# Optimization experiments

Hardware: AMD Instinct MI355X
Metric: run time of the kernel (lower is better)

The kernel has to match this reference:

```python
import jax, jax.numpy as jnp
import numpy as np

NEG_SLOPE = 0.2
MASK_FILL = -1e9

N, F_IN, K, F_OUT = 4096, 512, 8, 128


def setup_inputs() -> dict:
    key = jax.random.key(0)
    k1, k2, k3, k4, k5 = jax.random.split(key, 5)
    x = jax.random.normal(k1, (N, F_IN), dtype=jnp.float32)
    mask = jax.random.randint(k2, (N, N), 0, 2).astype(jnp.bool_)
    # ensure no fully-masked row (self loops)
    mask = mask | jnp.eye(N, dtype=jnp.bool_)
    # xavier-ish scaled params
    W = jax.random.normal(k3, (K * F_OUT, F_IN), dtype=jnp.float32) * (2.0 / (F_IN + K * F_OUT)) ** 0.5
    b = jnp.zeros((K * F_OUT,), dtype=jnp.float32)
    a_left = jax.random.normal(k4, (K, F_OUT), dtype=jnp.float32) * (2.0 / (1 + F_OUT)) ** 0.5
    a_right = jax.random.normal(k5, (K, F_OUT), dtype=jnp.float32) * (2.0 / (1 + F_OUT)) ** 0.5
    return {"x": x, "mask": mask, "W": W, "b": b, "a_left": a_left, "a_right": a_right}


def reference(x, mask, W, b, a_left, a_right):
    # Linear projection: (N, K*F') -> (N, K, F')
    h = (x @ W.T + b).reshape(x.shape[0], K, F_OUT)
    # Additive attention logits: e[k,n,m] = leaky_relu(a_left.h_n + a_right.h_m)
    left = jnp.einsum('nkf,kf->kn', h, a_left)    # (K, N)
    right = jnp.einsum('mkf,kf->km', h, a_right)  # (K, N)
    e = jax.nn.leaky_relu(left[:, :, None] + right[:, None, :], NEG_SLOPE)  # (K,N,N)
    # Mask out non-neighbors, softmax over neighbor axis m
    e = jnp.where(mask[None, :, :], e, MASK_FILL)
    a = jax.nn.softmax(e, axis=-1)  # (K, N, N)
    # Weighted aggregation (eq. 4) + ELU
    h_prime = jax.nn.elu(jnp.einsum('knm,mkf->nkf', a, h))  # (N, K, F')
    # Concat heads (eq. 5): (N, K*F')
    return h_prime.reshape(h_prime.shape[0], -1)
```

## Files before the change

### kernel.cpp

```cpp
#include <hip/hip_runtime.h>
#include <hip/hip_bf16.h>

typedef unsigned short u16;
typedef __attribute__((ext_vector_type(8))) short short8;
typedef __attribute__((ext_vector_type(2))) float f32x2;
typedef __attribute__((ext_vector_type(4))) float f32x4;
typedef __attribute__((ext_vector_type(16))) float f32x16;

#define N_NODES 4096
#define FIN 512
#define KH 8
#define FO 128
#define DM 1024
#define LOG2E 1.44269504088896340736f

__device__ __forceinline__ void gload16(const u16* g, u16* l) {
    __builtin_amdgcn_global_load_lds(
        (const __attribute__((address_space(1))) unsigned int*)g,
        (__attribute__((address_space(3))) unsigned int*)l,
        16, 0, 0);
}

__device__ __forceinline__ unsigned pk_bf16(float lo, float hi) {
    unsigned r;
    asm("v_cvt_pk_bf16_f32 %0, %1, %2" : "=v"(r) : "v"(lo), "v"(hi));
    return r;
}

__device__ __forceinline__ float pkmul_max(f32x2 a, f32x2 b) {
    f32x2 r;
    asm("v_pk_mul_f32 %0, %1, %2" : "=v"(r) : "v"(a), "v"(b));
    return fmaxf(r.x, r.y);
}

__global__ __launch_bounds__(256) void split_bf16(const float* __restrict__ src,
                                                  u16* __restrict__ hi,
                                                  u16* __restrict__ lo,
                                                  int n4) {
    int idx = blockIdx.x * 256 + threadIdx.x;
    if (idx >= n4) return;
    float4 v = ((const float4*)src)[idx];
    unsigned h01 = pk_bf16(v.x, v.y);
    unsigned h23 = pk_bf16(v.z, v.w);
    float hx = __uint_as_float(h01 << 16);
    float hy = __uint_as_float(h01 & 0xffff0000u);
    float hz = __uint_as_float(h23 << 16);
    float hw = __uint_as_float(h23 & 0xffff0000u);
    unsigned l01 = pk_bf16(v.x - hx, v.y - hy);
    unsigned l23 = pk_bf16(v.z - hz, v.w - hw);
    uint2 hv; hv.x = h01; hv.y = h23;
    uint2 lv; lv.x = l01; lv.y = l23;
    ((uint2*)hi)[idx] = hv;
    ((uint2*)lo)[idx] = lv;
}

__global__ __launch_bounds__(512) void gemm_mfma(const u16* __restrict__ Xh,
                                                 const u16* __restrict__ Xl,
                                                 const u16* __restrict__ Wh,
                                                 const u16* __restrict__ Wl,
                                                 const float* __restrict__ bias,
                                                 const float* __restrict__ aL,
                                                 const float* __restrict__ aR,
                                                 float2* __restrict__ C2,
                                                 unsigned* __restrict__ D2b,
                                                 u16* __restrict__ HbT) {
    const int khead = blockIdx.x;
    const int n0 = blockIdx.y * 128;
    const int tid = threadIdx.x;
    const int w = tid >> 6, lane = tid & 63;
    const int wr = w >> 1, wc = w & 1;
    const int c = lane & 31, half = lane >> 5;

    __shared__ u16 S[2][16384];

    const int sa = w >> 1;
    const int shv = w & 1;
    const int scl = lane & 3;
    const int ssw = ((lane >> 2) ^ (lane >> 4)) & 3;
    const int sgc = scl ^ ssw;
    const u16* gb; int growbase;
    if (sa == 0)      { gb = Xh; growbase = n0; }
    else if (sa == 1) { gb = Xl; growbase = n0; }
    else if (sa == 2) { gb = Wh; growbase = khead * 128; }
    else              { gb = Wl; growbase = khead * 128; }
    const u16* glb = gb + (size_t)(growbase + shv * 64 + (lane >> 2)) * FIN + sgc * 8;
    const int sldsoff = sa * 4096 + shv * 64 * 32;

    const int sw = ((c) ^ (c >> 2)) & 3;
    const int aoff = (wr * 32 + c) * 32;
    const int boff0 = 8192 + (wc * 64 + c) * 32;
    const int boff1 = 8192 + (wc * 64 + 32 + c) * 32;

    f32x16 acc0, acc1;
#pragma unroll
    for (int i = 0; i < 16; ++i) { acc0[i] = 0.f; acc1[i] = 0.f; }

#pragma unroll
    for (int i = 0; i < 4; ++i)
        gload16(glb + (size_t)i * 16 * FIN, &S[0][sldsoff + i * 512]);
    __syncthreads();

    int cur = 0;
    for (int kt = 0; kt < 16; ++kt) {
        if (kt < 15) {
            const u16* gsrc = glb + (kt + 1) * 32;
            u16* dst = &S[cur ^ 1][sldsoff];
#pragma unroll
            for (int i = 0; i < 4; ++i)
                gload16(gsrc + (size_t)i * 16 * FIN, dst + i * 512);
        }

        const u16* sp = S[cur];
        short8 ah[2], al8[2], bh[2][2], bl8[2][2];
#pragma unroll
        for (int ks = 0; ks < 2; ++ks) {
            int ch = ((ks * 2 + half) ^ sw) * 8;
            ah[ks]     = *(const short8*)&sp[aoff + ch];
            al8[ks]    = *(const short8*)&sp[4096 + aoff + ch];
            bh[0][ks]  = *(const short8*)&sp[boff0 + ch];
            bl8[0][ks] = *(const short8*)&sp[boff0 + 4096 + ch];
            bh[1][ks]  = *(const short8*)&sp[boff1 + ch];
            bl8[1][ks] = *(const short8*)&sp[boff1 + 4096 + ch];
        }
#pragma unroll
        for (int ks = 0; ks < 2; ++ks) {
            acc0 = __builtin_amdgcn_mfma_f32_32x32x16_bf16(ah[ks], bh[0][ks], acc0, 0, 0, 0);
            acc0 = __builtin_amdgcn_mfma_f32_32x32x16_bf16(ah[ks], bl8[0][ks], acc0, 0, 0, 0);
            acc0 = __builtin_amdgcn_mfma_f32_32x32x16_bf16(al8[ks], bh[0][ks], acc0, 0, 0, 0);
            acc1 = __builtin_amdgcn_mfma_f32_32x32x16_bf16(ah[ks], bh[1][ks], acc1, 0, 0, 0);
            acc1 = __builtin_amdgcn_mfma_f32_32x32x16_bf16(ah[ks], bl8[1][ks], acc1, 0, 0, 0);
            acc1 = __builtin_amdgcn_mfma_f32_32x32x16_bf16(al8[ks], bh[1][ks], acc1, 0, 0, 0);
        }
        __syncthreads();
        cur ^= 1;
    }

    const int fglob = khead * FO + wc * 64 + c;
    float b0 = bias[fglob], b1 = bias[fglob + 32];
#pragma unroll
    for (int r = 0; r < 16; ++r) { acc0[r] += b0; acc1[r] += b1; }

    float alv0 = aL[fglob], alv1 = aL[fglob + 32];
    float arv0 = aR[fglob], arv1 = aR[fglob + 32];
    float pl[16], pr[16];
#pragma unroll
    for (int r = 0; r < 16; ++r) {
        pl[r] = acc0[r] * alv0 + acc1[r] * alv1;
        pr[r] = acc0[r] * arv0 + acc1[r] * arv1;
    }
#pragma unroll
    for (int off = 1; off < 32; off <<= 1) {
#pragma unroll
        for (int r = 0; r < 16; ++r) {
            pl[r] += __shfl_xor(pl[r], off);
            pr[r] += __shfl_xor(pr[r], off);
        }
    }

    u16* T = &S[0][0];
    float* LRf = (float*)&S[0][0] + 9216;

    if (c == 0) {
#pragma unroll
        for (int r = 0; r < 16; ++r) {
            int node = wr * 32 + (r & 3) + 8 * (r >> 2) + 4 * half;
            LRf[(wc * 2 + 0) * 128 + node] = pl[r];
            LRf[(wc * 2 + 1) * 128 + node] = pr[r];
        }
    }

#pragma unroll
    for (int q = 0; q < 4; ++q) {
        int nb = wr * 32 + q * 8 + 4 * half;
        unsigned p00 = pk_bf16(acc0[q * 4 + 0], acc0[q * 4 + 1]);
        unsigned p01 = pk_bf16(acc0[q * 4 + 2], acc0[q * 4 + 3]);
        unsigned p10 = pk_bf16(acc1[q * 4 + 0], acc1[q * 4 + 1]);
        unsigned p11 = pk_bf16(acc1[q * 4 + 2], acc1[q * 4 + 3]);
        *(unsigned*)&T[(wc * 64 + c) * 136 + nb]      = p00;
        *(unsigned*)&T[(wc * 64 + c) * 136 + nb + 2]  = p01;
        *(unsigned*)&T[(wc * 64 + 32 + c) * 136 + nb]     = p10;
        *(unsigned*)&T[(wc * 64 + 32 + c) * 136 + nb + 2] = p11;
    }
    __syncthreads();

    if (wc == 0) {
        int node = wr * 32 + (lane & 31);
        if (lane < 32) {
            float L = (LRf[0 * 128 + node] + LRf[2 * 128 + node]) * LOG2E;
            float2 cv; cv.x = exp2f(L); cv.y = exp2f(0.2f * L);
            C2[(size_t)khead * N_NODES + n0 + node] = cv;
        } else {
            float R = (LRf[1 * 128 + node] + LRf[3 * 128 + node]) * LOG2E;
            D2b[(size_t)khead * N_NODES + n0 + node] = pk_bf16(exp2f(R), exp2f(0.2f * R));
        }
    }

    {
        int f = tid >> 2, q = tid & 3;
        const uint4* src = (const uint4*)&T[f * 136 + q * 32];
        uint4* dst = (uint4*)(HbT + (size_t)(khead * FO + f) * N_NODES + n0 + q * 32);
#pragma unroll
        for (int u = 0; u < 4; ++u) dst[u] = src[u];
    }
}

__global__ __launch_bounds__(256) void pack_mask(const int* __restrict__ mask,
                                                 unsigned long long* __restrict__ mb) {
    int gid = blockIdx.x * 256 + threadIdx.x;
    int wid = gid >> 6, lane = gid & 63;
    int v = mask[(size_t)wid * 64 + lane];
    unsigned long long bits = __ballot(v != 0);
    if (lane == 0) mb[wid] = bits;
}

__device__ __forceinline__ void pgen(f32x2 cc, uint4 a0v, uint4 a1v, uint4 b0v, uint4 b1v,
                                     unsigned long long bits, int kg,
                                     short8& A0, short8& A1) {
    unsigned m32a = (unsigned)(bits >> (kg * 8));
    unsigned m32b = (unsigned)(bits >> (kg * 8 + 32));
    unsigned dua[8] = {a0v.x, a0v.y, a0v.z, a0v.w, a1v.x, a1v.y, a1v.z, a1v.w};
    unsigned dub[8] = {b0v.x, b0v.y, b0v.z, b0v.w, b1v.x, b1v.y, b1v.z, b1v.w};
    float p0[8], p1[8];
#pragma unroll
    for (int v = 0; v < 8; ++v) {
        f32x2 dva; dva.x = __uint_as_float(dua[v] << 16);
        dva.y = __uint_as_float(dua[v] & 0xffff0000u);
        float pa = pkmul_max(cc, dva);
        unsigned sa2 = (unsigned)(((int)(m32a << (31 - v))) >> 31);
        p0[v] = __uint_as_float(__float_as_uint(pa) & sa2);
        f32x2 dvb; dvb.x = __uint_as_float(dub[v] << 16);
        dvb.y = __uint_as_float(dub[v] & 0xffff0000u);
        float pb = pkmul_max(cc, dvb);
        unsigned sb2 = (unsigned)(((int)(m32b << (31 - v))) >> 31);
        p1[v] = __uint_as_float(__float_as_uint(pb) & sb2);
    }
    union { unsigned u[4]; short8 s; } ua, ub;
#pragma unroll
    for (int vp = 0; vp < 4; ++vp) {
        ua.u[vp] = pk_bf16(p0[2 * vp], p0[2 * vp + 1]);
        ub.u[vp] = pk_bf16(p1[2 * vp], p1[2 * vp + 1]);
    }
    A0 = ua.s; A1 = ub.s;
}

__global__ __launch_bounds__(512, 4) void gat_attn(const u16* __restrict__ HbT,
                                                   const float2* __restrict__ C2,
                                                   const unsigned* __restrict__ D2b,
                                                   const unsigned long long* __restrict__ mb,
                                                   float* __restrict__ out) {
    const int blk = blockIdx.x;
    const int k = blk & 7;
    const int n0 = (blk >> 3) * 64;
    const int tid = threadIdx.x;
    const int w = tid >> 6, lane = tid & 63;
    const int g = w >> 2, wg = w & 3;
    const int fr = lane & 15, kg = lane >> 4;

    __shared__ u16 Ht[2][2][128 * 64];

    const int n_a = n0 + wg * 16 + fr;
    const float2 ccf = C2[(size_t)k * N_NODES + n_a];
    f32x2 cc; cc.x = ccf.x; cc.y = ccf.y;
    const unsigned long long* mrow = mb + (size_t)n_a * 64 + g * 32;

    f32x4 acc[9];
#pragma unroll
    for (int c = 0; c < 9; ++c) acc[c] = 0.f;

    const short o1 = (fr == 0) ? (short)0x3F80 : (short)0;
    const short8 ones = {o1, o1, o1, o1, o1, o1, o1, o1};

    const int fsub = lane >> 3;
    const int seg = ((lane & 7) ^ fsub) * 8;
    const u16* gstage = HbT + (size_t)(k * FO + wg * 32 + fsub) * N_NODES + g * 2048 + seg;
    u16* lb0 = &Ht[g][0][wg * 2048];
    u16* lb1 = &Ht[g][1][wg * 2048];

    const int frx = fr & 7;
    const int off0 = fr * 64 + (kg ^ frx) * 8;
    const int off1 = fr * 64 + ((kg + 4) ^ frx) * 8;

    const unsigned* D2k = D2b + (size_t)k * N_NODES + g * 2048 + kg * 8;

    uint4 dA0, dA1, dB0, dB1, eA0, eA1, eB0, eB1;
    unsigned long long bc, bn;
    dA0 = *(const uint4*)(D2k);      dA1 = *(const uint4*)(D2k + 4);
    dB0 = *(const uint4*)(D2k + 32); dB1 = *(const uint4*)(D2k + 36);
    bc = mrow[0];
    __builtin_amdgcn_sched_barrier(0);
#pragma unroll
    for (int j = 0; j < 4; ++j)
        gload16(gstage + (size_t)j * 8 * N_NODES, lb0 + j * 512);
    __builtin_amdgcn_sched_barrier(0);
#pragma unroll
    for (int j = 0; j < 4; ++j)
        gload16(gstage + 64 + (size_t)j * 8 * N_NODES, lb1 + j * 512);
    __builtin_amdgcn_sched_barrier(0);
    asm volatile("s_waitcnt vmcnt(4)" ::: "memory");
    __builtin_amdgcn_sched_barrier(0);
    __builtin_amdgcn_s_barrier();
    __builtin_amdgcn_sched_barrier(0);

#define ATTN_STEP(BUF, MT, DA0,DA1,DB0,DB1,BITS, NA0,NA1,NB0,NB1,NBITS)  do {          \
    short8 a0, a1;                                                                      \
    pgen(cc, DA0, DA1, DB0, DB1, BITS, kg, a0, a1);                                     \
    __builtin_amdgcn_sched_barrier(0);                                                  \
    { const unsigned* dnp = D2k + ((((MT) + 1) & 31) << 6);                             \
      NA0 = *(const uint4*)(dnp);      NA1 = *(const uint4*)(dnp + 4);                  \
      NB0 = *(const uint4*)(dnp + 32); NB1 = *(const uint4*)(dnp + 36);                 \
      NBITS = mrow[((MT) + 1) & 31]; }                                                  \
    __builtin_amdgcn_sched_barrier(0);                                                  \
    { const u16* hb = &Ht[g][BUF][0];                                                   \
      _Pragma("unroll")                                                                 \
      for (int c = 0; c < 8; ++c) {                                                     \
          short8 b0 = *(const short8*)(hb + c * 1024 + off0);                           \
          short8 b1 = *(const short8*)(hb + c * 1024 + off1);                           \
          acc[c] = __builtin_amdgcn_mfma_f32_16x16x32_bf16(a0, b0, acc[c], 0, 0, 0);    \
          acc[c] = __builtin_amdgcn_mfma_f32_16x16x32_bf16(a1, b1, acc[c], 0, 0, 0);    \
      }                                                                                 \
      acc[8] = __builtin_amdgcn_mfma_f32_16x16x32_bf16(a0, ones, acc[8], 0, 0, 0);      \
      acc[8] = __builtin_amdgcn_mfma_f32_16x16x32_bf16(a1, ones, acc[8], 0, 0, 0); }    \
    asm volatile("s_waitcnt lgkmcnt(0)" ::: "memory");                                  \
    __builtin_amdgcn_sched_barrier(0);                                                  \
    __builtin_amdgcn_s_barrier();                                                       \
    __builtin_amdgcn_sched_barrier(0);                                                  \
    { const u16* gs = gstage + ((((MT) + 2) & 31) << 6);                                \
      u16* lbs = (BUF) ? lb1 : lb0;                                                     \
      _Pragma("unroll")                                                                 \
      for (int j = 0; j < 4; ++j)                                                       \
          gload16(gs + (size_t)j * 8 * N_NODES, lbs + j * 512); }                       \
    __builtin_amdgcn_sched_barrier(0);                                                  \
    asm volatile("s_waitcnt vmcnt(9)" ::: "memory");                                    \
    __builtin_amdgcn_sched_barrier(0);                                                  \
    __builtin_amdgcn_s_barrier();                                                       \
    __builtin_amdgcn_sched_barrier(0);                                                  \
} while (0)

    for (int mt = 0; mt < 32; mt += 2) {
        ATTN_STEP(0, mt,     dA0, dA1, dB0, dB1, bc,  eA0, eA1, eB0, eB1, bn);
        ATTN_STEP(1, mt + 1, eA0, eA1, eB0, eB1, bn,  dA0, dA1, dB0, dB1, bc);
    }
#undef ATTN_STEP

    __syncthreads();

    float* cmb = (float*)&Ht[0][0][0];
    if (g == 1) {
        float* base = cmb + wg * (36 * 64);
#pragma unroll
        for (int c = 0; c < 9; ++c)
#pragma unroll
            for (int j = 0; j < 4; ++j) base[(c * 4 + j) * 64 + lane] = acc[c][j];
    }
    __syncthreads();
    if (g == 0) {
        const float* base = cmb + wg * (36 * 64);
#pragma unroll
        for (int c = 0; c < 9; ++c)
#pragma unroll
            for (int j = 0; j < 4; ++j) acc[c][j] += base[(c * 4 + j) * 64 + lane];

#pragma unroll
        for (int j = 0; j < 4; ++j) {
            float S = __shfl(acc[8][j], (lane & 48));
            float inv = 1.0f / S;
            int n_out = n0 + wg * 16 + kg * 4 + j;
            float* orow = out + (size_t)n_out * DM + k * FO + fr;
#pragma unroll
            for (int c = 0; c < 8; ++c) {
                float v = acc[c][j] * inv;
                float e = v > 0.f ? v : (__expf(v) - 1.0f);
                orow[c * 16] = e;
            }
        }
    }
}

extern "C" void kernel_launch(void* const* d_in, const int* in_sizes, int n_in,
                              void* d_out, int out_size, void* d_ws, size_t ws_size,
                              hipStream_t stream) {
    const float* x = (const float*)d_in[0];
    const int* mask = (const int*)d_in[1];
    const float* W = (const float*)d_in[2];
    const float* bias = (const float*)d_in[3];
    const float* aL = (const float*)d_in[4];
    const float* aR = (const float*)d_in[5];
    float* out = (float*)d_out;

    char* ws = (char*)d_ws;
    u16* Xh = (u16*)ws;   ws += (size_t)N_NODES * FIN * 2;
    u16* Xl = (u16*)ws;   ws += (size_t)N_NODES * FIN * 2;
    u16* Wh = (u16*)ws;   ws += (size_t)DM * FIN * 2;
    u16* Wl = (u16*)ws;   ws += (size_t)DM * FIN * 2;
    u16* HbT = (u16*)ws;  ws += (size_t)KH * FO * N_NODES * 2;
    float2* C2 = (float2*)ws;  ws += (size_t)KH * N_NODES * 8;
    unsigned* D2b = (unsigned*)ws; ws += (size_t)KH * N_NODES * 4;
    unsigned long long* mb = (unsigned long long*)ws;

    split_bf16<<<dim3(2048), dim3(256), 0, stream>>>(x, Xh, Xl, N_NODES * FIN / 4);
    split_bf16<<<dim3(512), dim3(256), 0, stream>>>(W, Wh, Wl, DM * FIN / 4);
    gemm_mfma<<<dim3(8, 32), dim3(512), 0, stream>>>(Xh, Xl, Wh, Wl, bias, aL, aR,
                                                     C2, D2b, HbT);
    pack_mask<<<dim3(65536), dim3(256), 0, stream>>>(mask, mb);
    gat_attn<<<dim3(512), dim3(512), 0, stream>>>(HbT, C2, D2b, mb, out);
}
```

Baseline: 131.7 us.

## Restructure attention loop to single-barrier double buffering with distance-one prefetch

Reworks the main attention loop so each half-step first issues the global-to-LDS load for the next tile into the other buffer, then computes on the current buffer, followed by one combined wait and a single barrier. This replaces the two-barrier, distance-two prefetch scheme. It also drops the inline-asm packed multiply and most sched_barriers so the compiler can schedule the probability generation freely. The goal is lower synchronisation overhead, at the cost of less load-latency slack per tile.

```diff
diff --git a/kernel.cpp b/kernel.cpp
--- a/kernel.cpp
+++ b/kernel.cpp
@@ -3,7 +3,6 @@
 
 typedef unsigned short u16;
 typedef __attribute__((ext_vector_type(8))) short short8;
-typedef __attribute__((ext_vector_type(2))) float f32x2;
 typedef __attribute__((ext_vector_type(4))) float f32x4;
 typedef __attribute__((ext_vector_type(16))) float f32x16;
 
@@ -25,12 +24,6 @@
     unsigned r;
     asm("v_cvt_pk_bf16_f32 %0, %1, %2" : "=v"(r) : "v"(lo), "v"(hi));
     return r;
-}
-
-__device__ __forceinline__ float pkmul_max(f32x2 a, f32x2 b) {
-    f32x2 r;
-    asm("v_pk_mul_f32 %0, %1, %2" : "=v"(r) : "v"(a), "v"(b));
-    return fmaxf(r.x, r.y);
 }
 
 __global__ __launch_bounds__(256) void split_bf16(const float* __restrict__ src,
@@ -213,36 +206,6 @@
     if (lane == 0) mb[wid] = bits;
 }
 
-__device__ __forceinline__ void pgen(f32x2 cc, uint4 a0v, uint4 a1v, uint4 b0v, uint4 b1v,
-                                     unsigned long long bits, int kg,
-                                     short8& A0, short8& A1) {
-    unsigned m32a = (unsigned)(bits >> (kg * 8));
-    unsigned m32b = (unsigned)(bits >> (kg * 8 + 32));
-    unsigned dua[8] = {a0v.x, a0v.y, a0v.z, a0v.w, a1v.x, a1v.y, a1v.z, a1v.w};
-    unsigned dub[8] = {b0v.x, b0v.y, b0v.z, b0v.w, b1v.x, b1v.y, b1v.z, b1v.w};
-    float p0[8], p1[8];
-#pragma unroll
-    for (int v = 0; v < 8; ++v) {
-        f32x2 dva; dva.x = __uint_as_float(dua[v] << 16);
-        dva.y = __uint_as_float(dua[v] & 0xffff0000u);
-        float pa = pkmul_max(cc, dva);
-        unsigned sa2 = (unsigned)(((int)(m32a << (31 - v))) >> 31);
-        p0[v] = __uint_as_float(__float_as_uint(pa) & sa2);
-        f32x2 dvb; dvb.x = __uint_as_float(dub[v] << 16);
-        dvb.y = __uint_as_float(dub[v] & 0xffff0000u);
-        float pb = pkmul_max(cc, dvb);
-        unsigned sb2 = (unsigned)(((int)(m32b << (31 - v))) >> 31);
-        p1[v] = __uint_as_float(__float_as_uint(pb) & sb2);
-    }
-    union { unsigned u[4]; short8 s; } ua, ub;
-#pragma unroll
-    for (int vp = 0; vp < 4; ++vp) {
-        ua.u[vp] = pk_bf16(p0[2 * vp], p0[2 * vp + 1]);
-        ub.u[vp] = pk_bf16(p1[2 * vp], p1[2 * vp + 1]);
-    }
-    A0 = ua.s; A1 = ub.s;
-}
-
 __global__ __launch_bounds__(512, 4) void gat_attn(const u16* __restrict__ HbT,
                                                    const float2* __restrict__ C2,
                                                    const unsigned* __restrict__ D2b,
@@ -260,8 +223,9 @@
 
     const int n_a = n0 + wg * 16 + fr;
     const float2 ccf = C2[(size_t)k * N_NODES + n_a];
-    f32x2 cc; cc.x = ccf.x; cc.y = ccf.y;
+    const float ccx = ccf.x, ccy = ccf.y;
     const unsigned long long* mrow = mb + (size_t)n_a * 64 + g * 32;
+    const int shA = kg * 8, shB = shA + 32;
 
     f32x4 acc[9];
 #pragma unroll
@@ -282,66 +246,83 @@
 
     const unsigned* D2k = D2b + (size_t)k * N_NODES + g * 2048 + kg * 8;
 
-    uint4 dA0, dA1, dB0, dB1, eA0, eA1, eB0, eB1;
-    unsigned long long bc, bn;
-    dA0 = *(const uint4*)(D2k);      dA1 = *(const uint4*)(D2k + 4);
-    dB0 = *(const uint4*)(D2k + 32); dB1 = *(const uint4*)(D2k + 36);
-    bc = mrow[0];
-    __builtin_amdgcn_sched_barrier(0);
+    uint4 dc0, dc1, dc2, dc3;
+    unsigned long long bc;
 #pragma unroll
     for (int j = 0; j < 4; ++j)
         gload16(gstage + (size_t)j * 8 * N_NODES, lb0 + j * 512);
-    __builtin_amdgcn_sched_barrier(0);
-#pragma unroll
-    for (int j = 0; j < 4; ++j)
-        gload16(gstage + 64 + (size_t)j * 8 * N_NODES, lb1 + j * 512);
-    __builtin_amdgcn_sched_barrier(0);
-    asm volatile("s_waitcnt vmcnt(4)" ::: "memory");
-    __builtin_amdgcn_sched_barrier(0);
+    dc0 = *(const uint4*)(D2k);      dc1 = *(const uint4*)(D2k + 4);
+    dc2 = *(const uint4*)(D2k + 32); dc3 = *(const uint4*)(D2k + 36);
+    bc = mrow[0];
+    asm volatile("s_waitcnt vmcnt(5)" ::: "memory");
     __builtin_amdgcn_s_barrier();
-    __builtin_amdgcn_sched_barrier(0);
-
-#define ATTN_STEP(BUF, MT, DA0,DA1,DB0,DB1,BITS, NA0,NA1,NB0,NB1,NBITS)  do {          \
-    short8 a0, a1;                                                                      \
-    pgen(cc, DA0, DA1, DB0, DB1, BITS, kg, a0, a1);                                     \
+
+#define ATTN_HALF(RBUF, SBUF, MT, DC0,DC1,DC2,DC3,BITS, DN0,DN1,DN2,DN3,NBITS) do {    \
+    const unsigned nxt = ((MT) + 1) & 31;                                               \
+    if ((MT) < 31) {                                                                    \
+        const u16* gs = gstage + ((size_t)nxt << 6);                                    \
+        _Pragma("unroll")                                                               \
+        for (int j = 0; j < 4; ++j)                                                     \
+            gload16(gs + (size_t)j * 8 * N_NODES, (SBUF) + j * 512);                    \
+    }                                                                                   \
+    { const unsigned* dnp = D2k + (nxt << 6);                                           \
+      DN0 = *(const uint4*)(dnp);      DN1 = *(const uint4*)(dnp + 4);                  \
+      DN2 = *(const uint4*)(dnp + 32); DN3 = *(const uint4*)(dnp + 36);                 \
+      NBITS = mrow[nxt]; }                                                              \
     __builtin_amdgcn_sched_barrier(0);                                                  \
-    { const unsigned* dnp = D2k + ((((MT) + 1) & 31) << 6);                             \
-      NA0 = *(const uint4*)(dnp);      NA1 = *(const uint4*)(dnp + 4);                  \
-      NB0 = *(const uint4*)(dnp + 32); NB1 = *(const uint4*)(dnp + 36);                 \
-      NBITS = mrow[((MT) + 1) & 31]; }                                                  \
-    __builtin_amdgcn_sched_barrier(0);                                                  \
-    { const u16* hb = &Ht[g][BUF][0];                                                   \
-      _Pragma("unroll")                                                                 \
-      for (int c = 0; c < 8; ++c) {                                                     \
-          short8 b0 = *(const short8*)(hb + c * 1024 + off0);                           \
-          short8 b1 = *(const short8*)(hb + c * 1024 + off1);                           \
-          acc[c] = __builtin_amdgcn_mfma_f32_16x16x32_bf16(a0, b0, acc[c], 0, 0, 0);    \
-          acc[c] = __builtin_amdgcn_mfma_f32_16x16x32_bf16(a1, b1, acc[c], 0, 0, 0);    \
-      }                                                                                 \
-      acc[8] = __builtin_amdgcn_mfma_f32_16x16x32_bf16(a0, ones, acc[8], 0, 0, 0);      \
-      acc[8] = __builtin_amdgcn_mfma_f32_16x16x32_bf16(a1, ones, acc[8], 0, 0, 0); }    \
+    {                                                                                   \
+        unsigned m32a = (unsigned)((BITS) >> shA);                                      \
+        unsigned m32b = (unsigned)((BITS) >> shB);                                      \
+        unsigned wa[8] = {DC0.x, DC0.y, DC0.z, DC0.w, DC1.x, DC1.y, DC1.z, DC1.w};      \
+        unsigned wb[8] = {DC2.x, DC2.y, DC2.z, DC2.w, DC3.x, DC3.y, DC3.z, DC3.w};      \
+        float p0[8], p1[8];                                                             \
+        _Pragma("unroll")                                                               \
+        for (int v = 0; v < 8; ++v) {                                                   \
+            float pa = fmaxf(ccx * __uint_as_float(wa[v] << 16),                        \
+                             ccy * __uint_as_float(wa[v] & 0xffff0000u));               \
+            unsigned sa2 = (unsigned)(((int)(m32a << (31 - v))) >> 31);                 \
+            p0[v] = __uint_as_float(__float_as_uint(pa) & sa2);                         \
+            float pb = fmaxf(ccx * __uint_as_float(wb[v] << 16),                        \
+                             ccy * __uint_as_float(wb[v] & 0xffff0000u));               \
+            unsigned sb2 = (unsigned)(((int)(m32b << (31 - v))) >> 31);                 \
+            p1[v] = __uint_as_float(__float_as_uint(pb) & sb2);                         \
+        }                                                                               \
+        union { unsigned u[4]; short8 s; } ua, ub;                                      \
+        _Pragma("unroll")                                                               \
+        for (int vp = 0; vp < 4; ++vp) {                                                \
+            ua.u[vp] = pk_bf16(p0[2 * vp], p0[2 * vp + 1]);                             \
+            ub.u[vp] = pk_bf16(p1[2 * vp], p1[2 * vp + 1]);                             \
+        }                                                                               \
+        short8 a0 = ua.s, a1 = ub.s;                                                    \
+        const u16* hb = (RBUF);                                                         \
+        _Pragma("unroll")                                                               \
+        for (int c = 0; c < 8; ++c) {                                                   \
+            short8 b0 = *(const short8*)(hb + c * 1024 + off0);                         \
+            short8 b1 = *(const short8*)(hb + c * 1024 + off1);                         \
+            acc[c] = __builtin_amdgcn_mfma_f32_16x16x32_bf16(a0, b0, acc[c], 0, 0, 0);  \
+            acc[c] = __builtin_amdgcn_mfma_f32_16x16x32_bf16(a1, b1, acc[c], 0, 0, 0);  \
+        }                                                                               \
+        acc[8] = __builtin_amdgcn_mfma_f32_16x16x32_bf16(a0, ones, acc[8], 0, 0, 0);    \
+        acc[8] = __builtin_amdgcn_mfma_f32_16x16x32_bf16(a1, ones, acc[8], 0, 0, 0);    \
+    }                                                                                   \
     asm volatile("s_waitcnt lgkmcnt(0)" ::: "memory");                                  \
-    __builtin_amdgcn_sched_barrier(0);                                                  \
+    asm volatile("s_waitcnt vmcnt(5)" ::: "memory");                                    \
     __builtin_amdgcn_s_barrier();                                                       \
-    __builtin_amdgcn_sched_barrier(0);                                                  \
-    { const u16* gs = gstage + ((((MT) + 2) & 31) << 6);                                \
-      u16* lbs = (BUF) ? lb1 : lb0;                                                     \
-      _Pragma("unroll")                                                                 \
-      for (int j = 0; j < 4; ++j)                                                       \
-          gload16(gs + (size_t)j * 8 * N_NODES, lbs + j * 512); }                       \
-    __builtin_amdgcn_sched_barrier(0);                                                  \
-    asm volatile("s_waitcnt vmcnt(9)" ::: "memory");                                    \
-    __builtin_amdgcn_sched_barrier(0);                                                  \
-    __builtin_amdgcn_s_barrier();                                                       \
-    __builtin_amdgcn_sched_barrier(0);                                                  \
 } while (0)
 
-    for (int mt = 0; mt < 32; mt += 2) {
-        ATTN_STEP(0, mt,     dA0, dA1, dB0, dB1, bc,  eA0, eA1, eB0, eB1, bn);
-        ATTN_STEP(1, mt + 1, eA0, eA1, eB0, eB1, bn,  dA0, dA1, dB0, dB1, bc);
-    }
-#undef ATTN_STEP
-
+    {
+        uint4 en0, en1, en2, en3;
+        unsigned long long bn;
+        const u16* rb0 = &Ht[g][0][0];
+        const u16* rb1 = &Ht[g][1][0];
+        for (int mt = 0; mt < 32; mt += 2) {
+            ATTN_HALF(rb0, lb1, mt,     dc0, dc1, dc2, dc3, bc, en0, en1, en2, en3, bn);
+            ATTN_HALF(rb1, lb0, mt + 1, en0, en1, en2, en3, bn, dc0, dc1, dc2, dc3, bc);
+        }
+    }
+#undef ATTN_HALF
+
+    asm volatile("s_waitcnt vmcnt(0)" ::: "memory");
     __syncthreads();
 
     float* cmb = (float*)&Ht[0][0][0];
```

Result: faster. 126.9 us (-3.7%).
